# Kernel tuning notes

Hardware: AMD Instinct MI355X
Metric: run time of the kernel (lower is better)

## Reference

```python
import jax, jax.numpy as jnp
import numpy as np

V, N, D, HID, F, HF, C, K = 2, 4096, 1024, 1800, 512, 128, 10, 10


def setup_inputs() -> dict:
    key = jax.random.key(0)
    ks = jax.random.split(key, 12)
    r = lambda k, s: jax.random.normal(k, s, jnp.float32) * 0.05
    return {
        'xs': jax.random.normal(ks[0], (V, N, D), jnp.float32),
        'enc_w1': r(ks[1], (V, D, HID)), 'enc_b1': jnp.zeros((V, HID), jnp.float32),
        'enc_w2': r(ks[2], (V, HID, F)), 'enc_b2': jnp.zeros((V, F), jnp.float32),
        'enc_W': r(ks[3], (V, F, F)),
        'dec_W1': r(ks[4], (V, F, F)),
        'dec_w1': r(ks[5], (V, F, HID)), 'dec_b1': jnp.zeros((V, HID), jnp.float32),
        'dec_w2': r(ks[6], (V, HID, D)), 'dec_b2': jnp.zeros((V, D), jnp.float32),
        'fc_w': r(ks[7], (F, HF)), 'fc_b': jnp.zeros((HF,), jnp.float32),
        'lc_w': r(ks[8], (F, C)), 'lc_b': jnp.zeros((C,), jnp.float32),
    }


def knn_graph(x):
    # brute-force squared euclidean distances [N, N]
    sq = jnp.sum(x * x, axis=1)
    dists = sq[:, None] - 2.0 * (x @ x.T) + sq[None, :]
    # K smallest distances per row (includes self, removed below)
    _, idx = jax.lax.top_k(-dists, K)  # [N, K]
    n = x.shape[0]
    g = jnp.zeros((n, n), x.dtype).at[jnp.arange(n)[:, None], idx].set(1.0)
    g = g * (1.0 - jnp.eye(n, dtype=x.dtype))  # zero diagonal
    g = jnp.maximum(g, g.T)                    # symmetrize
    return g


def comp(g):
    # D^-1/2 (A + I) D^-1/2
    gh = g + jnp.eye(g.shape[0], dtype=g.dtype)
    d = gh.sum(axis=1) ** -0.5  # deg >= 1 so no inf
    return d[:, None] * gh * d[None, :]


def _per_view(x, ew1, eb1, ew2, eb2, eW, dW1, dw1, db1, dw2, db2, fc_w, fc_b, lc_w, lc_b):
    g = jax.lax.stop_gradient(knn_graph(x))
    s = jax.lax.stop_gradient(comp(g))
    # Encoder
    o1 = jnp.tanh((s @ x) @ ew1 + eb1)
    z = jnp.tanh((s @ o1) @ ew2 + eb2)
    a = jax.nn.sigmoid((z @ eW) @ z.T)
    # contrastive heads
    h = z @ fc_w + fc_b
    h = h / jnp.linalg.norm(h, axis=1, keepdims=True)
    q = jax.nn.softmax(z @ lc_w + lc_b, axis=1)
    # Decoder
    h1 = jnp.tanh(z @ dW1)
    h11 = jnp.tanh((s @ h1) @ dw1 + db1)
    xr = jnp.tanh((s @ h11) @ dw2 + db2)
    return h, q, xr, z, g, a


def reference(xs, enc_w1, enc_b1, enc_w2, enc_b2, enc_W, dec_W1, dec_w1, dec_b1,
              dec_w2, dec_b2, fc_w, fc_b, lc_w, lc_b):
    fn = jax.vmap(_per_view, in_axes=(0,) * 11 + (None,) * 4)
    hs, qs, xrs, zs, gs, ars = fn(xs, enc_w1, enc_b1, enc_w2, enc_b2, enc_W,
                                  dec_W1, dec_w1, dec_b1, dec_w2, dec_b2,
                                  fc_w, fc_b, lc_w, lc_b)
    return hs, qs, xrs, zs, gs, ars
```

## Files before the change

### kernel.cpp

```cpp
#include <hip/hip_runtime.h>
#include <math.h>
#include <stdint.h>

typedef uint16_t u16;
typedef __attribute__((ext_vector_type(8))) short short8;
typedef __attribute__((ext_vector_type(8))) __bf16 bf16x8;
typedef __attribute__((ext_vector_type(4))) float f32x4;
union V8 { short8 s; bf16x8 b; };

__device__ __align__(256) char g_scratch[234881024];

#define NBR_CAP 2048

__device__ inline float bf2f(u16 u){ return __uint_as_float(((uint32_t)u)<<16); }
__device__ inline u16 f2bf(float f){
  uint32_t x = __float_as_uint(f);
  uint32_t r = (x + 0x7FFFu + ((x>>16)&1u)) >> 16;
  return (u16)r;
}

__global__ __launch_bounds__(256) void zero_k(f32x4* __restrict__ p, size_t n4){
  size_t i = (size_t)blockIdx.x*256 + threadIdx.x;
  size_t stride = (size_t)gridDim.x*256;
  f32x4 z = {0.f,0.f,0.f,0.f};
  for (; i < n4; i += stride) p[i] = z;
}

__global__ __launch_bounds__(256) void sq_kernel(const float* __restrict__ x,
                                                 float* __restrict__ sqf){
  int wid = threadIdx.x >> 6, lane = threadIdx.x & 63;
  int row = blockIdx.x*4 + wid;
  const float* xr = x + (size_t)row*1024;
  double acc = 0.0;
  for (int k = lane; k < 1024; k += 64){ float v = xr[k]; acc += (double)v*(double)v; }
  for (int o = 32; o > 0; o >>= 1) acc += __shfl_down(acc, o);
  if (lane == 0) sqf[row] = (float)acc;
}

__global__ __launch_bounds__(256) void split_k(const float* __restrict__ x, u16* __restrict__ h,
                                               u16* __restrict__ l, int n){
  int i = blockIdx.x*256 + threadIdx.x;
  int stride = gridDim.x*256;
  for (; i < n; i += stride){
    float v = x[i];
    u16 hh = f2bf(v);
    h[i] = hh;
    if (l) l[i] = f2bf(v - bf2f(hh));
  }
}

__global__ __launch_bounds__(256) void tsplit_k(const float* __restrict__ w, u16* __restrict__ th,
                                                u16* __restrict__ tl, int K, int N){
  __shared__ float t[64][65];
  const int kb = blockIdx.y*64, nb = blockIdx.x*64;
  const int x = threadIdx.x & 63, y = threadIdx.x >> 6;
  for (int yy = y; yy < 64; yy += 4){
    int k = kb + yy, n = nb + x;
    t[yy][x] = (k < K && n < N) ? w[(size_t)k*N + n] : 0.f;
  }
  __syncthreads();
  for (int yy = y; yy < 64; yy += 4){
    int n = nb + yy, k = kb + x;
    if (n < N && k < K){
      float v = t[x][yy];
      u16 hh = f2bf(v);
      th[(size_t)n*K + k] = hh;
      tl[(size_t)n*K + k] = f2bf(v - bf2f(hh));
    }
  }
}

template<int NS, int EPI>
__global__ __launch_bounds__(256) void gemm_bt(
    const u16* __restrict__ A0, const u16* __restrict__ A1,
    const u16* __restrict__ B0, const u16* __restrict__ B1,
    const float* __restrict__ bias, const float* __restrict__ sqf,
    float* __restrict__ C, int M, int N, int K)
{
  __shared__ u16 As[NS][128][40];
  __shared__ u16 Bs[NS][128][40];
  const int tid = threadIdx.x;
  const int rowBase = blockIdx.y*128, colBase = blockIdx.x*128;
  const int wid = tid>>6, lane = tid&63;
  const int wr = (wid>>1)*64, wc = (wid&1)*64;
  const int lrow = lane&15, lq = lane>>4;

  f32x4 acc[4][4];
  #pragma unroll
  for (int m=0;m<4;++m)
    #pragma unroll
    for (int n=0;n<4;++n) acc[m][n] = (f32x4){0.f,0.f,0.f,0.f};

  const u16* Ap[2] = {A0, A1};
  const u16* Bp[2] = {B0, B1};

  for (int k0 = 0; k0 < K; k0 += 32){
    #pragma unroll
    for (int s=0; s<NS; ++s){
      #pragma unroll
      for (int p=0;p<2;++p){
        int idx = p*256 + tid;
        int r = idx>>2, c8 = (idx&3)<<3;
        int gk = k0 + c8;
        short8 v = {0,0,0,0,0,0,0,0};
        if (gk < K) v = *(const short8*)(Ap[s] + (size_t)(rowBase+r)*K + gk);
        *(short8*)&As[s][r][c8] = v;
      }
      #pragma unroll
      for (int p=0;p<2;++p){
        int idx = p*256 + tid;
        int r = idx>>2, c8 = (idx&3)<<3;
        int gn = colBase + r, gk = k0 + c8;
        short8 v = {0,0,0,0,0,0,0,0};
        if (gk < K && gn < N) v = *(const short8*)(Bp[s] + (size_t)gn*K + gk);
        *(short8*)&Bs[s][r][c8] = v;
      }
    }
    __syncthreads();
    V8 af[NS][4], bfr[NS][4];
    #pragma unroll
    for (int s=0;s<NS;++s)
      #pragma unroll
      for (int m=0;m<4;++m)
        af[s][m].s = *(const short8*)&As[s][wr + m*16 + lrow][lq<<3];
    #pragma unroll
    for (int s=0;s<NS;++s)
      #pragma unroll
      for (int n=0;n<4;++n)
        bfr[s][n].s = *(const short8*)&Bs[s][wc + n*16 + lrow][lq<<3];
    #pragma unroll
    for (int m=0;m<4;++m)
      #pragma unroll
      for (int n=0;n<4;++n){
        acc[m][n] = __builtin_amdgcn_mfma_f32_16x16x32_bf16(af[0][m].b, bfr[0][n].b, acc[m][n], 0,0,0);
        if (NS == 2){
          acc[m][n] = __builtin_amdgcn_mfma_f32_16x16x32_bf16(af[NS-1][m].b, bfr[0][n].b, acc[m][n], 0,0,0);
          acc[m][n] = __builtin_amdgcn_mfma_f32_16x16x32_bf16(af[0][m].b, bfr[NS-1][n].b, acc[m][n], 0,0,0);
        }
      }
    __syncthreads();
  }

  #pragma unroll
  for (int m=0;m<4;++m)
    #pragma unroll
    for (int n=0;n<4;++n)
      #pragma unroll
      for (int r=0;r<4;++r){
        int row = rowBase + wr + m*16 + lq*4 + r;
        int col = colBase + wc + n*16 + lrow;
        if (col < N){
          float c = acc[m][n][r];
          if (EPI == 3) c = sqf[row] + sqf[col] - 2.0f*c;
          if (bias) c += bias[col];
          if (EPI == 1) c = tanhf(c);
          if (EPI == 2) c = 1.0f/(1.0f + expf(-c));
          C[(size_t)row*N + col] = c;
        }
      }
}

template<int EPI>
__global__ __launch_bounds__(256) void sgemm_k(
    const float* __restrict__ A, const float* __restrict__ B,
    const float* __restrict__ bias, float* __restrict__ C, int M, int N, int K)
{
  __shared__ float As[64][17];
  __shared__ float Bs[16][65];
  const int tid = threadIdx.x;
  const int tx = tid & 15, ty = tid >> 4;
  const int rowBase = blockIdx.y*64, colBase = blockIdx.x*64;
  float acc[4][4] = {{0.f}};
  for (int k0 = 0; k0 < K; k0 += 16){
    #pragma unroll
    for (int p = 0; p < 4; ++p){
      int idx = p*256 + tid;
      int r = idx >> 4, kk = idx & 15;
      int gk = k0 + kk;
      As[r][kk] = (gk < K) ? A[(size_t)(rowBase+r)*K + gk] : 0.f;
    }
    #pragma unroll
    for (int p = 0; p < 4; ++p){
      int idx = p*256 + tid;
      int k = idx >> 6, c = idx & 63;
      int gk = k0 + k, gc = colBase + c;
      Bs[k][c] = (gk < K && gc < N) ? B[(size_t)gk*N + gc] : 0.f;
    }
    __syncthreads();
    #pragma unroll
    for (int k = 0; k < 16; ++k){
      float a[4], b[4];
      #pragma unroll
      for (int i=0;i<4;++i) a[i] = As[ty*4+i][k];
      #pragma unroll
      for (int j=0;j<4;++j) b[j] = Bs[k][tx*4+j];
      #pragma unroll
      for (int i=0;i<4;++i)
        #pragma unroll
        for (int j=0;j<4;++j) acc[i][j] = fmaf(a[i], b[j], acc[i][j]);
    }
    __syncthreads();
  }
  #pragma unroll
  for (int i=0;i<4;++i){
    int row = rowBase + ty*4 + i;
    #pragma unroll
    for (int j=0;j<4;++j){
      int col = colBase + tx*4 + j;
      if (col < N){
        float c = acc[i][j];
        if (bias) c += bias[col];
        if (EPI == 1) c = tanhf(c);
        C[(size_t)row*N + col] = c;
      }
    }
  }
}

__global__ __launch_bounds__(256) void knn_select(const float* __restrict__ dists,
                                                  int* __restrict__ cand, int* __restrict__ candc){
  const int row = blockIdx.x, tid = threadIdx.x;
  __shared__ float drow[4096];
  __shared__ float rv[256]; __shared__ int ri[256];
  __shared__ float d10s;
  const float* dr = dists + (size_t)row*4096;
  for (int j = tid; j < 4096; j += 256) drow[j] = dr[j];
  __syncthreads();
  for (int t = 0; t < 10; ++t){
    float bv = 3.4e38f; int bi = 0x7FFFFFFF;
    for (int j = tid; j < 4096; j += 256){
      float v = drow[j];
      if (v < bv || (v == bv && j < bi)){ bv = v; bi = j; }
    }
    rv[tid] = bv; ri[tid] = bi;
    __syncthreads();
    for (int s = 128; s > 0; s >>= 1){
      if (tid < s){
        float ov = rv[tid+s]; int oi = ri[tid+s];
        if (ov < rv[tid] || (ov == rv[tid] && oi < ri[tid])){ rv[tid] = ov; ri[tid] = oi; }
      }
      __syncthreads();
    }
    if (tid == 0){ drow[ri[0]] = 3.4e38f; if (t == 9) d10s = rv[0]; }
    __syncthreads();
  }
  const float thr = d10s + 2.0f;
  if (tid < 64){
    int lane = tid;
    int cnt = 0;
    for (int base = 0; base < 4096; base += 64){
      bool p = dr[base+lane] <= thr;
      unsigned long long mask = __ballot(p);
      if (p){
        int pos = __popcll(mask & ((1ull<<lane)-1ull));
        if (cnt + pos < 96) cand[(size_t)row*96 + cnt + pos] = base + lane;
      }
      cnt += __popcll(mask);
    }
    if (lane == 0) candc[row] = cnt < 96 ? cnt : 96;
  }
}

__global__ __launch_bounds__(256) void knn_rank32(const float* __restrict__ x,
    const int* __restrict__ cand, const int* __restrict__ candc,
    int* __restrict__ nbrK, int* __restrict__ nbrKc)
{
  const int row = blockIdx.x, tid = threadIdx.x;
  const int wid = tid>>6, lane = tid&63;
  __shared__ float xi[1024];
  __shared__ float cd[96];
  __shared__ float sqi_sh;
  const float* xr = x + (size_t)row*1024;
  for (int k = tid; k < 1024; k += 256) xi[k] = xr[k];
  __syncthreads();
  if (wid == 0){
    float a = 0.f;
    #pragma unroll
    for (int t = 0; t < 16; ++t){ float v = xi[lane + 64*t]; a = fmaf(v, v, a); }
    a += __shfl_xor(a, 16); a += __shfl_xor(a, 32);
    a += __shfl_xor(a, 8);  a += __shfl_xor(a, 4);
    a += __shfl_xor(a, 2);  a += __shfl_xor(a, 1);
    if (lane == 0) sqi_sh = a;
  }
  __syncthreads();
  const float sqi = sqi_sh;
  const int cnt = candc[row];
  for (int s = wid; s < cnt; s += 4){
    int c = cand[(size_t)row*96 + s];
    const float* xc = x + (size_t)c*1024;
    float ad = 0.f, aq = 0.f;
    #pragma unroll
    for (int t = 0; t < 16; ++t){
      int k = lane + 64*t;
      float v = xc[k];
      ad = fmaf(xi[k], v, ad);
      aq = fmaf(v, v, aq);
    }
    ad += __shfl_xor(ad, 16); ad += __shfl_xor(ad, 32);
    ad += __shfl_xor(ad, 8);  ad += __shfl_xor(ad, 4);
    ad += __shfl_xor(ad, 2);  ad += __shfl_xor(ad, 1);
    aq += __shfl_xor(aq, 16); aq += __shfl_xor(aq, 32);
    aq += __shfl_xor(aq, 8);  aq += __shfl_xor(aq, 4);
    aq += __shfl_xor(aq, 2);  aq += __shfl_xor(aq, 1);
    if (lane == 0) cd[s] = (sqi - 2.0f*ad) + aq;
  }
  __syncthreads();
  if (tid == 0){
    int m = 0;
    int lim = cnt < 10 ? cnt : 10;
    for (int t = 0; t < lim; ++t){
      float bd = 3.4e38f; int bs = 0;
      for (int s = 0; s < cnt; ++s){
        if (cd[s] < bd){ bd = cd[s]; bs = s; }
      }
      cd[bs] = 3.4e38f;
      int j = cand[(size_t)row*96 + bs];
      if (j != row && m < 10){ nbrK[row*10 + m] = j; ++m; }
    }
    nbrKc[row] = m;
  }
}

__global__ __launch_bounds__(64) void scatter_k(const int* __restrict__ nbrK, const int* __restrict__ nbrKc,
                                                float* __restrict__ g){
  int row = blockIdx.x, t = threadIdx.x;
  int m = nbrKc[row];
  if (t < m){
    int j = nbrK[row*10 + t];
    g[(size_t)row*4096 + j] = 1.0f;
    g[(size_t)j*4096 + row] = 1.0f;
  }
}

__global__ __launch_bounds__(64) void build_lists(const float* __restrict__ g, int* __restrict__ nbrl,
                                                  int* __restrict__ nbrc, float* __restrict__ dinv){
  int row = blockIdx.x, lane = threadIdx.x;
  const float* gr = g + (size_t)row*4096;
  int cnt = 0;
  for (int base = 0; base < 4096; base += 64){
    bool p = gr[base+lane] != 0.f;
    unsigned long long mask = __ballot(p);
    if (p){
      int pos = __popcll(mask & ((1ull<<lane)-1ull));
      if (cnt + pos < NBR_CAP) nbrl[(size_t)row*NBR_CAP + cnt + pos] = base + lane;
    }
    cnt += __popcll(mask);
  }
  if (lane == 0){
    nbrc[row] = cnt < NBR_CAP ? cnt : NBR_CAP;
    dinv[row] = 1.0f/sqrtf((float)(cnt + 1));
  }
}

__global__ __launch_bounds__(256) void spmm_k(const float* __restrict__ X, const int* __restrict__ nbrl,
    const int* __restrict__ nbrc, const float* __restrict__ dinv, float* __restrict__ out, int W){
  const int row = blockIdx.y;
  const int lane = threadIdx.x & 63;
  const int sl = threadIdx.x >> 6;
  const int col4 = blockIdx.x*256 + lane*4;
  __shared__ int li[NBR_CAP]; __shared__ float lv[NBR_CAP];
  __shared__ f32x4 red[4][64];
  const int cnt = nbrc[row];
  for (int t = threadIdx.x; t < cnt; t += 256){
    int j = nbrl[(size_t)row*NBR_CAP + t];
    li[t] = j; lv[t] = dinv[j];
  }
  __syncthreads();
  const float di = dinv[row];
  f32x4 p = {0.f,0.f,0.f,0.f};
  if (col4 + 3 < W){
    for (int s = sl; s < cnt; s += 4){
      f32x4 xv = *(const f32x4*)(X + (size_t)li[s]*W + col4);
      p += lv[s]*xv;
    }
    if (sl == 0){
      f32x4 xv = *(const f32x4*)(X + (size_t)row*W + col4);
      p += di*xv;
    }
  } else if (col4 < W){
    #pragma unroll
    for (int e = 0; e < 4; ++e){
      int c = col4 + e;
      if (c < W){
        float a = 0.f;
        for (int s = sl; s < cnt; s += 4) a = fmaf(lv[s], X[(size_t)li[s]*W + c], a);
        if (sl == 0) a = fmaf(di, X[(size_t)row*W + c], a);
        p[e] = a;
      }
    }
  }
  red[sl][lane] = p;
  __syncthreads();
  if (sl == 0 && col4 < W){
    f32x4 acc = red[0][lane] + red[1][lane] + red[2][lane] + red[3][lane];
    acc = di*acc;
    #pragma unroll
    for (int e = 0; e < 4; ++e){
      int c = col4 + e;
      if (c < W) out[(size_t)row*W + c] = acc[e];
    }
  }
}

__global__ __launch_bounds__(64) void q_kernel(const float* __restrict__ z, const float* __restrict__ lcw,
                                               const float* __restrict__ lcb, float* __restrict__ qs){
  int row = blockIdx.x, lane = threadIdx.x;
  __shared__ float ls[10];
  const float* zr = z + (size_t)row*512;
  for (int c = 0; c < 10; ++c){
    float a = 0.f;
    for (int k = lane; k < 512; k += 64) a += zr[k]*lcw[k*10 + c];
    for (int o = 32; o > 0; o >>= 1) a += __shfl_down(a, o);
    if (lane == 0) ls[c] = a + lcb[c];
  }
  __syncthreads();
  if (lane == 0){
    float m = ls[0];
    for (int c = 1; c < 10; ++c) m = fmaxf(m, ls[c]);
    float sum = 0.f, e[10];
    for (int c = 0; c < 10; ++c){ e[c] = expf(ls[c]-m); sum += e[c]; }
    for (int c = 0; c < 10; ++c) qs[(size_t)row*10 + c] = e[c]/sum;
  }
}

__global__ __launch_bounds__(64) void hnorm_k(const float* __restrict__ hp, float* __restrict__ hs){
  int row = blockIdx.x, lane = threadIdx.x;
  const float* hr = hp + (size_t)row*128;
  float v0 = hr[lane], v1 = hr[lane+64];
  float a = v0*v0 + v1*v1;
  for (int o = 32; o > 0; o >>= 1) a += __shfl_down(a, o);
  float nrm = sqrtf(__shfl(a, 0));
  hs[(size_t)row*128 + lane]      = v0/nrm;
  hs[(size_t)row*128 + lane + 64] = v1/nrm;
}

extern "C" void kernel_launch(void* const* d_in, const int* in_sizes, int n_in,
                              void* d_out, int out_size, void* d_ws, size_t ws_size,
                              hipStream_t stream)
{
  const float* xs  = (const float*)d_in[0];
  const float* ew1 = (const float*)d_in[1];
  const float* eb1 = (const float*)d_in[2];
  const float* ew2 = (const float*)d_in[3];
  const float* eb2 = (const float*)d_in[4];
  const float* eWp = (const float*)d_in[5];
  const float* dW1 = (const float*)d_in[6];
  const float* dw1 = (const float*)d_in[7];
  const float* db1 = (const float*)d_in[8];
  const float* dw2 = (const float*)d_in[9];
  const float* db2 = (const float*)d_in[10];
  const float* fcw = (const float*)d_in[11];
  const float* fcb = (const float*)d_in[12];
  const float* lcw = (const float*)d_in[13];
  const float* lcb = (const float*)d_in[14];

  float* out = (float*)d_out;
  const size_t HS0 = 0;
  const size_t QS0 = HS0 + (size_t)2*4096*128;
  const size_t XR0 = QS0 + (size_t)2*4096*10;
  const size_t ZS0 = XR0 + (size_t)2*4096*1024;
  const size_t GS0 = ZS0 + (size_t)2*4096*512;
  const size_t AR0 = GS0 + (size_t)2*4096*4096;

  void* sp = nullptr;
  hipGetSymbolAddress(&sp, HIP_SYMBOL(g_scratch));
  if (!sp) return;
  char* ws = (char*)sp;

  float* dists = (float*)(ws + 0);
  u16* GAH = (u16*)(ws + 0);
  u16* GAL = (u16*)(ws + 14745600);
  u16* GWH = (u16*)(ws + 29491200);
  u16* GWL = (u16*)(ws + 33177600);
  u16* ZH  = (u16*)(ws + 36864000);
  u16* ZL  = (u16*)(ws + 41058304);
  u16* WH  = (u16*)(ws + 45252608);
  u16* WL  = (u16*)(ws + 49446912);

  float* o1    = (float*)(ws + 67108864);
  u16* XH = (u16*)(ws + 67108864);
  float* so1   = (float*)(ws + 96600064);
  float* sx    = (float*)(ws + 126091264);
  float* sh1   = (float*)(ws + 142868480);
  float* zw    = (float*)(ws + 151257088);
  float* h1    = (float*)(ws + 159645696);
  float* hpre  = (float*)(ws + 168034304);
  float* sqf   = (float*)(ws + 170164224);
  int* cand    = (int*)(ws + 170180608);
  int* candc   = (int*)(ws + 171753472);
  int* nbrK    = (int*)(ws + 171769856);
  int* nbrKc   = (int*)(ws + 171933696);
  int* nbrl    = (int*)(ws + 171950080);
  int* nbrc    = (int*)(ws + 205504512);
  float* dinv  = (float*)(ws + 205520896);
  float* h11   = o1;
  float* sh11  = so1;

  zero_k<<<2048,256,0,stream>>>((f32x4*)(out + GS0), (size_t)2*4096*4096/4);

  for (int v = 0; v < 2; ++v){
    const float* x    = xs  + (size_t)v*4096*1024;
    const float* w1   = ew1 + (size_t)v*1024*1800;
    const float* b1   = eb1 + (size_t)v*1800;
    const float* w2   = ew2 + (size_t)v*1800*512;
    const float* b2   = eb2 + (size_t)v*512;
    const float* We   = eWp + (size_t)v*512*512;
    const float* dWv  = dW1 + (size_t)v*512*512;
    const float* dw1v = dw1 + (size_t)v*512*1800;
    const float* db1v = db1 + (size_t)v*1800;
    const float* dw2v = dw2 + (size_t)v*1800*1024;
    const float* db2v = db2 + (size_t)v*1024;
    float* hs_o = out + HS0 + (size_t)v*4096*128;
    float* qs_o = out + QS0 + (size_t)v*4096*10;
    float* xr_o = out + XR0 + (size_t)v*4096*1024;
    float* zs_o = out + ZS0 + (size_t)v*4096*512;
    float* gs_o = out + GS0 + (size_t)v*4096*4096;
    float* ar_o = out + AR0 + (size_t)v*4096*4096;

    sq_kernel<<<1024,256,0,stream>>>(x, sqf);
    split_k<<<2048,256,0,stream>>>(x, XH, nullptr, 4096*1024);
    gemm_bt<1,3><<<dim3(32,32),256,0,stream>>>(XH,nullptr,XH,nullptr,nullptr,sqf,dists,4096,4096,1024);
    knn_select<<<4096,256,0,stream>>>(dists, cand, candc);
    knn_rank32<<<4096,256,0,stream>>>(x, cand, candc, nbrK, nbrKc);
    scatter_k<<<4096,64,0,stream>>>(nbrK, nbrKc, gs_o);
    build_lists<<<4096,64,0,stream>>>(gs_o, nbrl, nbrc, dinv);

    spmm_k<<<dim3(4,4096),256,0,stream>>>(x, nbrl, nbrc, dinv, sx, 1024);
    split_k<<<2048,256,0,stream>>>(sx, GAH, GAL, 4096*1024);
    tsplit_k<<<dim3(29,16),256,0,stream>>>(w1, GWH, GWL, 1024, 1800);
    gemm_bt<2,1><<<dim3(15,32),256,0,stream>>>(GAH,GAL,GWH,GWL,b1,nullptr,o1,4096,1800,1024);
    spmm_k<<<dim3(8,4096),256,0,stream>>>(o1, nbrl, nbrc, dinv, so1, 1800);
    split_k<<<2048,256,0,stream>>>(so1, GAH, GAL, 4096*1800);
    tsplit_k<<<dim3(8,29),256,0,stream>>>(w2, GWH, GWL, 1800, 512);
    gemm_bt<2,1><<<dim3(4,32),256,0,stream>>>(GAH,GAL,GWH,GWL,b2,nullptr,zs_o,4096,512,1800);

    split_k<<<2048,256,0,stream>>>(zs_o, ZH, ZL, 4096*512);
    tsplit_k<<<dim3(8,8),256,0,stream>>>(We, GWH, GWL, 512, 512);
    gemm_bt<2,0><<<dim3(4,32),256,0,stream>>>(ZH,ZL,GWH,GWL,nullptr,nullptr,zw,4096,512,512);
    split_k<<<2048,256,0,stream>>>(zw, WH, WL, 4096*512);
    gemm_bt<2,2><<<dim3(32,32),256,0,stream>>>(WH,WL,ZH,ZL,nullptr,nullptr,ar_o,4096,4096,512);

    sgemm_k<0><<<dim3(2,64),256,0,stream>>>(zs_o,fcw,fcb,hpre,4096,128,512);
    hnorm_k<<<4096,64,0,stream>>>(hpre, hs_o);
    q_kernel<<<4096,64,0,stream>>>(zs_o, lcw, lcb, qs_o);

    tsplit_k<<<dim3(8,8),256,0,stream>>>(dWv, GWH, GWL, 512, 512);
    gemm_bt<2,1><<<dim3(4,32),256,0,stream>>>(ZH,ZL,GWH,GWL,nullptr,nullptr,h1,4096,512,512);
    spmm_k<<<dim3(2,4096),256,0,stream>>>(h1, nbrl, nbrc, dinv, sh1, 512);
    split_k<<<2048,256,0,stream>>>(sh1, GAH, GAL, 4096*512);
    tsplit_k<<<dim3(29,8),256,0,stream>>>(dw1v, GWH, GWL, 512, 1800);
    gemm_bt<2,1><<<dim3(15,32),256,0,stream>>>(GAH,GAL,GWH,GWL,db1v,nullptr,h11,4096,1800,512);
    spmm_k<<<dim3(8,4096),256,0,stream>>>(h11, nbrl, nbrc, dinv, sh11, 1800);
    split_k<<<2048,256,0,stream>>>(sh11, GAH, GAL, 4096*1800);
    tsplit_k<<<dim3(16,29),256,0,stream>>>(dw2v, GWH, GWL, 1800, 1024);
    gemm_bt<2,1><<<dim3(8,32),256,0,stream>>>(GAH,GAL,GWH,GWL,db2v,nullptr,xr_o,4096,1024,1800);
  }
}
```

Before: 3.001 ms.

## Load GEMM tiles directly into LDS with XOR swizzle and padded operands

Replaces the register-staged global-to-shared copies in the bf16 split GEMM with global_load_lds direct-to-LDS transfers, using an XOR swizzle on the unpadded 32-wide shared tiles to avoid bank conflicts. To drop the per-load bounds checks, the split kernels now write operands zero-padded so K is a multiple of 32 and N is a multiple of 128, and the scratch offsets are enlarged to fit. This removes VGPR staging and branch overhead in the GEMM main loop. The cost is extra padding work in the split passes and reliance on exact padded layouts.

```diff
diff --git a/kernel.cpp b/kernel.cpp
--- a/kernel.cpp
+++ b/kernel.cpp
@@ -17,6 +17,11 @@
   uint32_t x = __float_as_uint(f);
   uint32_t r = (x + 0x7FFFu + ((x>>16)&1u)) >> 16;
   return (u16)r;
+}
+
+__device__ inline void gload16(const u16* g, u16* l){
+  __builtin_amdgcn_global_load_lds((const __attribute__((address_space(1))) uint32_t*)g,
+                                   (__attribute__((address_space(3))) uint32_t*)l, 16, 0, 0);
 }
 
 __global__ __launch_bounds__(256) void zero_k(f32x4* __restrict__ p, size_t n4){
@@ -37,20 +42,19 @@
   if (lane == 0) sqf[row] = (float)acc;
 }
 
-__global__ __launch_bounds__(256) void split_k(const float* __restrict__ x, u16* __restrict__ h,
-                                               u16* __restrict__ l, int n){
-  int i = blockIdx.x*256 + threadIdx.x;
-  int stride = gridDim.x*256;
-  for (; i < n; i += stride){
-    float v = x[i];
-    u16 hh = f2bf(v);
-    h[i] = hh;
-    if (l) l[i] = f2bf(v - bf2f(hh));
-  }
-}
-
-__global__ __launch_bounds__(256) void tsplit_k(const float* __restrict__ w, u16* __restrict__ th,
-                                                u16* __restrict__ tl, int K, int N){
+__global__ __launch_bounds__(256) void split_pad(const float* __restrict__ x, u16* __restrict__ h,
+                                                 u16* __restrict__ l, int K, int Kp){
+  int row = blockIdx.y;
+  int c = blockIdx.x*256 + threadIdx.x;
+  if (c >= Kp) return;
+  float v = (c < K) ? x[(size_t)row*K + c] : 0.f;
+  u16 hh = f2bf(v);
+  h[(size_t)row*Kp + c] = hh;
+  if (l) l[(size_t)row*Kp + c] = f2bf(v - bf2f(hh));
+}
+
+__global__ __launch_bounds__(256) void tsplit_pad(const float* __restrict__ w, u16* __restrict__ th,
+                                                  u16* __restrict__ tl, int K, int N, int Kp, int Npad){
   __shared__ float t[64][65];
   const int kb = blockIdx.y*64, nb = blockIdx.x*64;
   const int x = threadIdx.x & 63, y = threadIdx.x >> 6;
@@ -61,11 +65,11 @@
   __syncthreads();
   for (int yy = y; yy < 64; yy += 4){
     int n = nb + yy, k = kb + x;
-    if (n < N && k < K){
+    if (n < Npad && k < Kp){
       float v = t[x][yy];
       u16 hh = f2bf(v);
-      th[(size_t)n*K + k] = hh;
-      tl[(size_t)n*K + k] = f2bf(v - bf2f(hh));
+      th[(size_t)n*Kp + k] = hh;
+      tl[(size_t)n*Kp + k] = f2bf(v - bf2f(hh));
     }
   }
 }
@@ -75,16 +79,26 @@
     const u16* __restrict__ A0, const u16* __restrict__ A1,
     const u16* __restrict__ B0, const u16* __restrict__ B1,
     const float* __restrict__ bias, const float* __restrict__ sqf,
-    float* __restrict__ C, int M, int N, int K)
+    float* __restrict__ C, int M, int N, int Kp)
 {
-  __shared__ u16 As[NS][128][40];
-  __shared__ u16 Bs[NS][128][40];
+  __shared__ u16 As[NS][128][32];
+  __shared__ u16 Bs[NS][128][32];
   const int tid = threadIdx.x;
   const int rowBase = blockIdx.y*128, colBase = blockIdx.x*128;
   const int wid = tid>>6, lane = tid&63;
   const int wr = (wid>>1)*64, wc = (wid&1)*64;
   const int lrow = lane&15, lq = lane>>4;
 
+  int srow[2], scol[2];
+  #pragma unroll
+  for (int p=0;p<2;++p){
+    int slot = p*256 + tid;
+    srow[p] = slot>>2;
+    scol[p] = (slot&3) ^ (srow[p]&3);
+  }
+  const int loff0 = (wid*64)*8;
+  const int loff1 = (256 + wid*64)*8;
+
   f32x4 acc[4][4];
   #pragma unroll
   for (int m=0;m<4;++m)
@@ -94,40 +108,32 @@
   const u16* Ap[2] = {A0, A1};
   const u16* Bp[2] = {B0, B1};
 
-  for (int k0 = 0; k0 < K; k0 += 32){
-    #pragma unroll
-    for (int s=0; s<NS; ++s){
-      #pragma unroll
-      for (int p=0;p<2;++p){
-        int idx = p*256 + tid;
-        int r = idx>>2, c8 = (idx&3)<<3;
-        int gk = k0 + c8;
-        short8 v = {0,0,0,0,0,0,0,0};
-        if (gk < K) v = *(const short8*)(Ap[s] + (size_t)(rowBase+r)*K + gk);
-        *(short8*)&As[s][r][c8] = v;
-      }
-      #pragma unroll
-      for (int p=0;p<2;++p){
-        int idx = p*256 + tid;
-        int r = idx>>2, c8 = (idx&3)<<3;
-        int gn = colBase + r, gk = k0 + c8;
-        short8 v = {0,0,0,0,0,0,0,0};
-        if (gk < K && gn < N) v = *(const short8*)(Bp[s] + (size_t)gn*K + gk);
-        *(short8*)&Bs[s][r][c8] = v;
-      }
+  for (int k0 = 0; k0 < Kp; k0 += 32){
+    #pragma unroll
+    for (int s=0;s<NS;++s){
+      u16* al = &As[s][0][0];
+      u16* bl = &Bs[s][0][0];
+      gload16(Ap[s] + (size_t)(rowBase + srow[0])*Kp + (k0 + scol[0]*8), al + loff0);
+      gload16(Ap[s] + (size_t)(rowBase + srow[1])*Kp + (k0 + scol[1]*8), al + loff1);
+      gload16(Bp[s] + (size_t)(colBase + srow[0])*Kp + (k0 + scol[0]*8), bl + loff0);
+      gload16(Bp[s] + (size_t)(colBase + srow[1])*Kp + (k0 + scol[1]*8), bl + loff1);
     }
     __syncthreads();
     V8 af[NS][4], bfr[NS][4];
     #pragma unroll
     for (int s=0;s<NS;++s)
       #pragma unroll
-      for (int m=0;m<4;++m)
-        af[s][m].s = *(const short8*)&As[s][wr + m*16 + lrow][lq<<3];
+      for (int m=0;m<4;++m){
+        int r = wr + m*16 + lrow;
+        af[s][m].s = *(const short8*)(&As[s][0][0] + r*32 + ((lq ^ (r&3))<<3));
+      }
     #pragma unroll
     for (int s=0;s<NS;++s)
       #pragma unroll
-      for (int n=0;n<4;++n)
-        bfr[s][n].s = *(const short8*)&Bs[s][wc + n*16 + lrow][lq<<3];
+      for (int n=0;n<4;++n){
+        int r = wc + n*16 + lrow;
+        bfr[s][n].s = *(const short8*)(&Bs[s][0][0] + r*32 + ((lq ^ (r&3))<<3));
+      }
     #pragma unroll
     for (int m=0;m<4;++m)
       #pragma unroll
@@ -469,13 +475,13 @@
 
   float* dists = (float*)(ws + 0);
   u16* GAH = (u16*)(ws + 0);
-  u16* GAL = (u16*)(ws + 14745600);
-  u16* GWH = (u16*)(ws + 29491200);
-  u16* GWL = (u16*)(ws + 33177600);
-  u16* ZH  = (u16*)(ws + 36864000);
-  u16* ZL  = (u16*)(ws + 41058304);
-  u16* WH  = (u16*)(ws + 45252608);
-  u16* WL  = (u16*)(ws + 49446912);
+  u16* GAL = (u16*)(ws + 14942208);
+  u16* GWH = (u16*)(ws + 29884416);
+  u16* GWL = (u16*)(ws + 34078720);
+  u16* ZH  = (u16*)(ws + 38273024);
+  u16* ZL  = (u16*)(ws + 42467328);
+  u16* WH  = (u16*)(ws + 46661632);
+  u16* WL  = (u16*)(ws + 50855936);
 
   float* o1    = (float*)(ws + 67108864);
   u16* XH = (u16*)(ws + 67108864);
@@ -518,7 +524,7 @@
     float* ar_o = out + AR0 + (size_t)v*4096*4096;
 
     sq_kernel<<<1024,256,0,stream>>>(x, sqf);
-    split_k<<<2048,256,0,stream>>>(x, XH, nullptr, 4096*1024);
+    split_pad<<<dim3(4,4096),256,0,stream>>>(x, XH, nullptr, 1024, 1024);
     gemm_bt<1,3><<<dim3(32,32),256,0,stream>>>(XH,nullptr,XH,nullptr,nullptr,sqf,dists,4096,4096,1024);
     knn_select<<<4096,256,0,stream>>>(dists, cand, candc);
     knn_rank32<<<4096,256,0,stream>>>(x, cand, candc, nbrK, nbrKc);
@@ -526,33 +532,33 @@
     build_lists<<<4096,64,0,stream>>>(gs_o, nbrl, nbrc, dinv);
 
     spmm_k<<<dim3(4,4096),256,0,stream>>>(x, nbrl, nbrc, dinv, sx, 1024);
-    split_k<<<2048,256,0,stream>>>(sx, GAH, GAL, 4096*1024);
-    tsplit_k<<<dim3(29,16),256,0,stream>>>(w1, GWH, GWL, 1024, 1800);
+    split_pad<<<dim3(4,4096),256,0,stream>>>(sx, GAH, GAL, 1024, 1024);
+    tsplit_pad<<<dim3(30,16),256,0,stream>>>(w1, GWH, GWL, 1024, 1800, 1024, 1920);
     gemm_bt<2,1><<<dim3(15,32),256,0,stream>>>(GAH,GAL,GWH,GWL,b1,nullptr,o1,4096,1800,1024);
     spmm_k<<<dim3(8,4096),256,0,stream>>>(o1, nbrl, nbrc, dinv, so1, 1800);
-    split_k<<<2048,256,0,stream>>>(so1, GAH, GAL, 4096*1800);
-    tsplit_k<<<dim3(8,29),256,0,stream>>>(w2, GWH, GWL, 1800, 512);
-    gemm_bt<2,1><<<dim3(4,32),256,0,stream>>>(GAH,GAL,GWH,GWL,b2,nullptr,zs_o,4096,512,1800);
-
-    split_k<<<2048,256,0,stream>>>(zs_o, ZH, ZL, 4096*512);
-    tsplit_k<<<dim3(8,8),256,0,stream>>>(We, GWH, GWL, 512, 512);
+    split_pad<<<dim3(8,4096),256,0,stream>>>(so1, GAH, GAL, 1800, 1824);
+    tsplit_pad<<<dim3(8,29),256,0,stream>>>(w2, GWH, GWL, 1800, 512, 1824, 512);
+    gemm_bt<2,1><<<dim3(4,32),256,0,stream>>>(GAH,GAL,GWH,GWL,b2,nullptr,zs_o,4096,512,1824);
+
+    split_pad<<<dim3(2,4096),256,0,stream>>>(zs_o, ZH, ZL, 512, 512);
+    tsplit_pad<<<dim3(8,8),256,0,stream>>>(We, GWH, GWL, 512, 512, 512, 512);
     gemm_bt<2,0><<<dim3(4,32),256,0,stream>>>(ZH,ZL,GWH,GWL,nullptr,nullptr,zw,4096,512,512);
-    split_k<<<2048,256,0,stream>>>(zw, WH, WL, 4096*512);
+    split_pad<<<dim3(2,4096),256,0,stream>>>(zw, WH, WL, 512, 512);
     gemm_bt<2,2><<<dim3(32,32),256,0,stream>>>(WH,WL,ZH,ZL,nullptr,nullptr,ar_o,4096,4096,512);
 
     sgemm_k<0><<<dim3(2,64),256,0,stream>>>(zs_o,fcw,fcb,hpre,4096,128,512);
     hnorm_k<<<4096,64,0,stream>>>(hpre, hs_o);
     q_kernel<<<4096,64,0,stream>>>(zs_o, lcw, lcb, qs_o);
 
-    tsplit_k<<<dim3(8,8),256,0,stream>>>(dWv, GWH, GWL, 512, 512);
+    tsplit_pad<<<dim3(8,8),256,0,stream>>>(dWv, GWH, GWL, 512, 512, 512, 512);
     gemm_bt<2,1><<<dim3(4,32),256,0,stream>>>(ZH,ZL,GWH,GWL,nullptr,nullptr,h1,4096,512,512);
     spmm_k<<<dim3(2,4096),256,0,stream>>>(h1, nbrl, nbrc, dinv, sh1, 512);
-    split_k<<<2048,256,0,stream>>>(sh1, GAH, GAL, 4096*512);
-    tsplit_k<<<dim3(29,8),256,0,stream>>>(dw1v, GWH, GWL, 512, 1800);
+    split_pad<<<dim3(2,4096),256,0,stream>>>(sh1, GAH, GAL, 512, 512);
+    tsplit_pad<<<dim3(30,8),256,0,stream>>>(dw1v, GWH, GWL, 512, 1800, 512, 1920);
     gemm_bt<2,1><<<dim3(15,32),256,0,stream>>>(GAH,GAL,GWH,GWL,db1v,nullptr,h11,4096,1800,512);
     spmm_k<<<dim3(8,4096),256,0,stream>>>(h11, nbrl, nbrc, dinv, sh11, 1800);
-    split_k<<<2048,256,0,stream>>>(sh11, GAH, GAL, 4096*1800);
-    tsplit_k<<<dim3(16,29),256,0,stream>>>(dw2v, GWH, GWL, 1800, 1024);
-    gemm_bt<2,1><<<dim3(8,32),256,0,stream>>>(GAH,GAL,GWH,GWL,db2v,nullptr,xr_o,4096,1024,1800);
-  }
-}
+    split_pad<<<dim3(8,4096),256,0,stream>>>(sh11, GAH, GAL, 1800, 1824);
+    tsplit_pad<<<dim3(16,29),256,0,stream>>>(dw2v, GWH, GWL, 1800, 1024, 1824, 1024);
+    gemm_bt<2,1><<<dim3(8,32),256,0,stream>>>(GAH,GAL,GWH,GWL,db2v,nullptr,xr_o,4096,1024,1824);
+  }
+}
```

Result: faster. 2.568 ms (-14.4%).
